# Performance work log

Measured on AMD Instinct MI355X. Metric: run time of the kernel, lower is better.

## Reference

```python
import jax, jax.numpy as jnp
import numpy as np

N_NODES = 50000
N_EDGES = 600000
IN_F = 128
OUT_F = 128
SMALL = max(IN_F // 10, 1)  # floor(128/10) = 12
D_K = np.sqrt(SMALL).astype(np.float32)


def setup_inputs() -> dict:
    key = jax.random.key(0)
    ks = jax.random.split(key, 10)
    node_data = jax.random.normal(ks[0], (N_NODES, IN_F), dtype=jnp.float32)
    src = jax.random.randint(ks[1], (N_EDGES,), 0, N_NODES, dtype=jnp.int32)
    dst = jax.random.randint(ks[2], (N_EDGES,), 0, N_NODES, dtype=jnp.int32)
    s_q = 1.0 / np.sqrt(IN_F)
    Wq = jax.random.uniform(ks[3], (SMALL, IN_F), jnp.float32, -s_q, s_q)
    bq = jax.random.uniform(ks[4], (SMALL,), jnp.float32, -s_q, s_q)
    Wk = jax.random.uniform(ks[5], (SMALL, IN_F), jnp.float32, -s_q, s_q)
    bk = jax.random.uniform(ks[6], (SMALL,), jnp.float32, -s_q, s_q)
    W1 = jax.random.uniform(ks[7], (OUT_F, IN_F), jnp.float32, -s_q, s_q)
    W2 = jax.random.uniform(ks[8], (OUT_F, IN_F), jnp.float32, -s_q, s_q)
    b2 = jax.random.uniform(ks[9], (OUT_F,), jnp.float32, -s_q, s_q)
    return {"node_data": node_data, "src": src, "dst": dst,
            "Wq": Wq, "bq": bq, "Wk": Wk, "bk": bk,
            "W1": W1, "W2": W2, "b2": b2}


def reference(node_data, src, dst, Wq, bq, Wk, bk, W1, W2, b2):
    N = node_data.shape[0]
    # dgl.add_self_loop: append (i, i) for every node -> each dst has >= 1 edge
    loops = jnp.arange(N, dtype=src.dtype)
    s = jnp.concatenate([src, loops])
    d = jnp.concatenate([dst, loops])

    # query = Tanh(Linear), key = Linear  (shapes [N, SMALL])
    q = jnp.tanh(node_data @ Wq.T + bq)
    k = node_data @ Wk.T + bk

    # per-edge score: sum(query[src] * key[dst]) / sqrt(small)
    scores = jnp.sum(q[s] * k[d], axis=1) / D_K  # [E]

    # softmax over incoming edges of each dst node (segment softmax)
    seg_max = jax.ops.segment_max(scores, d, num_segments=N)
    w = jnp.exp(scores - seg_max[d])
    seg_sum = jax.ops.segment_sum(w, d, num_segments=N)
    w = w / seg_sum[d]  # [E]

    # weighted scatter-aggregate of src node inputs -> [N, IN_F]
    att = jax.ops.segment_sum(w[:, None] * node_data[s], d, num_segments=N)

    # DeepSetLayer: layer1(node_data) + layer2(node attention)
    x = node_data @ W1.T + (att @ W2.T + b2)
    # per-row L2 ('fro' over dim=1) normalization, then ReLU
    x = x / jnp.linalg.norm(x, axis=1, keepdims=True)
    return jax.nn.relu(x)
```

## Files before the change

kernel.cpp:

```cpp
#include <hip/hip_runtime.h>
#include <hip/hip_bf16.h>
#include <math.h>
#include <stdint.h>


#define IN_F 128
#define SMALL 12
#define QK_PAD 16
#define BUCKET 64

typedef __attribute__((ext_vector_type(8))) _Float16 half8;
typedef __attribute__((ext_vector_type(8))) unsigned short ushort8;
typedef __attribute__((ext_vector_type(4))) float f32x4;
typedef __attribute__((ext_vector_type(2))) float floatx2;

__device__ __forceinline__ float dot12(const float* __restrict__ qrow,
                                       float4 c0, float4 c1, float4 c2) {
    float4 a = ((const float4*)qrow)[0];
    float4 b = ((const float4*)qrow)[1];
    float4 c = ((const float4*)qrow)[2];
    return a.x*c0.x + a.y*c0.y + a.z*c0.z + a.w*c0.w
         + b.x*c1.x + b.y*c1.y + b.z*c1.z + b.w*c1.w
         + c.x*c2.x + c.y*c2.y + c.z*c2.z + c.w*c2.w;
}

__device__ __forceinline__ half8 ld_h8(const float* p) {
    float4 x0 = *(const float4*)p;
    float4 x1 = *(const float4*)(p + 4);
    half8 a;
    a[0] = (_Float16)x0.x; a[1] = (_Float16)x0.y;
    a[2] = (_Float16)x0.z; a[3] = (_Float16)x0.w;
    a[4] = (_Float16)x1.x; a[5] = (_Float16)x1.y;
    a[6] = (_Float16)x1.z; a[7] = (_Float16)x1.w;
    return a;
}

__global__ __launch_bounds__(256) void prep_kernel(
    const float* __restrict__ nd,
    const float* __restrict__ Wq, const float* __restrict__ bq,
    const float* __restrict__ Wk, const float* __restrict__ bk,
    const int* __restrict__ src, const int* __restrict__ dst,
    const float* __restrict__ W1, const float* __restrict__ W2,
    float* __restrict__ q, float* __restrict__ kf,
    unsigned short* __restrict__ ndb, unsigned char* __restrict__ nd8,
    int* __restrict__ cnt, unsigned short* __restrict__ esrc,
    unsigned short* __restrict__ Wc,
    int N, int E, int NBQK, int NBCNT)
{
    int t = threadIdx.x;
    int b = blockIdx.x;

    if (b < NBQK) {
        int wv = t >> 6;
        int lane = t & 63;
        int col = lane & 15;
        int quad = lane >> 4;
        int tbase = b * 64 + wv * 16;

        int arow = tbase + col;
        int rowc = (arow < N) ? arow : (N - 1);
        const float* ap = nd + (size_t)rowc * IN_F + quad * 8;
        unsigned short* np = ndb + (size_t)arow * IN_F + quad * 8;
        unsigned char* n8p = nd8 + (size_t)arow * IN_F + quad * 8;

        const float* w0 = ((col < 12) ? (Wq + (size_t)col * IN_F)
                                      : (Wk + (size_t)(col - 12) * IN_F)) + quad * 8;
        const float* w1 = Wk + (size_t)((col < 8) ? (col + 4) : 4) * IN_F + quad * 8;
        bool hasw1 = (col < 8);

        half8 zero = {};
        f32x4 acc0 = (f32x4)0.f, acc1 = (f32x4)0.f;
#pragma unroll
        for (int ks = 0; ks < 4; ks++) {
            int k0 = ks * 32;
            float4 x0 = *(const float4*)(ap + k0);
            float4 x1 = *(const float4*)(ap + k0 + 4);
            half8 a;
            a[0] = (_Float16)x0.x; a[1] = (_Float16)x0.y;
            a[2] = (_Float16)x0.z; a[3] = (_Float16)x0.w;
            a[4] = (_Float16)x1.x; a[5] = (_Float16)x1.y;
            a[6] = (_Float16)x1.z; a[7] = (_Float16)x1.w;
            if (arow < N) {
                *(half8*)(np + k0) = a;
                int p0 = __builtin_amdgcn_cvt_pk_fp8_f32(x0.x, x0.y, 0, false);
                p0 = __builtin_amdgcn_cvt_pk_fp8_f32(x0.z, x0.w, p0, true);
                int p1 = __builtin_amdgcn_cvt_pk_fp8_f32(x1.x, x1.y, 0, false);
                p1 = __builtin_amdgcn_cvt_pk_fp8_f32(x1.z, x1.w, p1, true);
                uint2 pv; pv.x = (unsigned)p0; pv.y = (unsigned)p1;
                *(uint2*)(n8p + k0) = pv;
            }
            half8 bb0 = ld_h8(w0 + k0);
            half8 bb1 = hasw1 ? ld_h8(w1 + k0) : zero;
            acc0 = __builtin_amdgcn_mfma_f32_16x16x32_f16(a, bb0, acc0, 0, 0, 0);
            acc1 = __builtin_amdgcn_mfma_f32_16x16x32_f16(a, bb1, acc1, 0, 0, 0);
        }
        float bias0 = (col < 12) ? bq[col] : bk[col - 12];
        float bias1 = (col < 8) ? bk[col + 4] : 0.f;
#pragma unroll
        for (int r = 0; r < 4; r++) {
            int node = tbase + quad * 4 + r;
            if (node < N) {
                float v0 = acc0[r] + bias0;
                if (col < 12) q[(size_t)node * QK_PAD + col] = tanhf(v0);
                else          kf[(size_t)node * QK_PAD + (col - 12)] = v0;
                if (hasw1)    kf[(size_t)node * QK_PAD + col + 4] = acc1[r] + bias1;
            }
        }
    } else if (b < NBQK + NBCNT) {
        int ET = E + N;
        int stride = NBCNT * 256;
        for (int i = (b - NBQK) * 256 + t; i < ET; i += stride) {
            int d, s;
            if (i < E) { d = dst[i]; s = src[i]; }
            else       { d = i - E; s = d; }
            int pos = atomicAdd(&cnt[d], 1);
            if (pos < BUCKET)
                esrc[(size_t)d * BUCKET + pos] = (unsigned short)s;
        }
    } else {
        int idx = (b - NBQK - NBCNT) * 256 + t;
        int f = idx >> 8, k = idx & 255;
        float v = (k < 128) ? W1[f * 128 + k] : W2[f * 128 + (k - 128)];
        ((_Float16*)Wc)[idx] = (_Float16)v;
    }
}

__global__ __launch_bounds__(256) void attn_kernel(
    const unsigned short* __restrict__ ndb, const unsigned char* __restrict__ nd8,
    const float* __restrict__ q,
    const float* __restrict__ kf,
    const int* __restrict__ cnt, const unsigned short* __restrict__ esrc,
    void* __restrict__ attv, int att16, int N)
{
    const float INVDK = 0.28867513459481287f;
    int t = threadIdx.x;
    int lane = t & 63;
    int l16 = lane & 15;
    int gbase = lane & 48;
    int wid = blockIdx.x * 16 + (t >> 4);
    if (wid >= N) return;

    int start = wid * BUCKET;
    int deg = cnt[wid];
    if (deg > BUCKET) deg = BUCKET;

    const float4* kp = (const float4*)(kf + (size_t)wid * QK_PAD);
    float4 c0 = kp[0], c1 = kp[1], c2 = kp[2];

    float acc[8];
#pragma unroll
    for (int j = 0; j < 8; j++) acc[j] = 0.f;
    float inv;

    const unsigned short* nb = ndb + l16 * 8;
    const unsigned char* nb8 = nd8 + l16 * 8;

#define ACCUM(hv, ww) do {                                                    \
        acc[0] += (ww) * (float)(hv)[0]; acc[1] += (ww) * (float)(hv)[1];     \
        acc[2] += (ww) * (float)(hv)[2]; acc[3] += (ww) * (float)(hv)[3];     \
        acc[4] += (ww) * (float)(hv)[4]; acc[5] += (ww) * (float)(hv)[5];     \
        acc[6] += (ww) * (float)(hv)[6]; acc[7] += (ww) * (float)(hv)[7];     \
    } while (0)

#define ACCUMQ(pv, ww) do {                                                   \
        floatx2 f0 = __builtin_amdgcn_cvt_pk_f32_fp8((int)(pv).x, false);     \
        floatx2 f1 = __builtin_amdgcn_cvt_pk_f32_fp8((int)(pv).x, true);      \
        floatx2 f2 = __builtin_amdgcn_cvt_pk_f32_fp8((int)(pv).y, false);     \
        floatx2 f3 = __builtin_amdgcn_cvt_pk_f32_fp8((int)(pv).y, true);      \
        acc[0] += (ww) * f0[0]; acc[1] += (ww) * f0[1];                       \
        acc[2] += (ww) * f1[0]; acc[3] += (ww) * f1[1];                       \
        acc[4] += (ww) * f2[0]; acc[5] += (ww) * f2[1];                       \
        acc[6] += (ww) * f3[0]; acc[7] += (ww) * f3[1]; } while (0)

#define LOAD8Q(pfx, id)                                                       \
    uint2 pfx##0 = *(const uint2*)(nb8 + (size_t)(id)[0] * IN_F);             \
    uint2 pfx##1 = *(const uint2*)(nb8 + (size_t)(id)[1] * IN_F);             \
    uint2 pfx##2 = *(const uint2*)(nb8 + (size_t)(id)[2] * IN_F);             \
    uint2 pfx##3 = *(const uint2*)(nb8 + (size_t)(id)[3] * IN_F);             \
    uint2 pfx##4 = *(const uint2*)(nb8 + (size_t)(id)[4] * IN_F);             \
    uint2 pfx##5 = *(const uint2*)(nb8 + (size_t)(id)[5] * IN_F);             \
    uint2 pfx##6 = *(const uint2*)(nb8 + (size_t)(id)[6] * IN_F);             \
    uint2 pfx##7 = *(const uint2*)(nb8 + (size_t)(id)[7] * IN_F)

#define SHFL8(wsrc, base)                                                     \
    do { _Pragma("unroll")                                                    \
         for (int _i = 0; _i < 8; _i++) wa[_i] = __shfl((wsrc), gbase | ((base) + _i)); } while (0)

#define ACCUM8Q(pfx) do {                                                     \
        ACCUMQ(pfx##0, wa[0]); ACCUMQ(pfx##1, wa[1]);                         \
        ACCUMQ(pfx##2, wa[2]); ACCUMQ(pfx##3, wa[3]);                         \
        ACCUMQ(pfx##4, wa[4]); ACCUMQ(pfx##5, wa[5]);                         \
        ACCUMQ(pfx##6, wa[6]); ACCUMQ(pfx##7, wa[7]); } while (0)

    if (deg <= 32) {
        ushort8 pk0 = *(const ushort8*)(esrc + start);
        ushort8 pk1 = *(const ushort8*)(esrc + start + 8);

        int id0[8];
#pragma unroll
        for (int i = 0; i < 8; i++) id0[i] = (i < deg) ? (int)pk0[i] : 0;
        LOAD8Q(v, id0);

        int si = (int)esrc[start + l16];
        float sc = -INFINITY;
        if (l16 < deg)
            sc = dot12(q + (size_t)si * QK_PAD, c0, c1, c2) * INVDK;
        float sc1 = -INFINITY;
        if (deg > 16) {
            int si1 = (int)esrc[start + 16 + l16];
            if (16 + l16 < deg)
                sc1 = dot12(q + (size_t)si1 * QK_PAD, c0, c1, c2) * INVDK;
        }
        float m = fmaxf(sc, sc1);
#pragma unroll
        for (int o = 8; o > 0; o >>= 1) m = fmaxf(m, __shfl_xor(m, o));
        float w  = (l16 < deg)      ? __expf(sc - m)  : 0.f;
        float w1 = (16 + l16 < deg) ? __expf(sc1 - m) : 0.f;
        float ls = w + w1;
#pragma unroll
        for (int o = 8; o > 0; o >>= 1) ls += __shfl_xor(ls, o);
        inv = 1.f / ls;

        int id1[8];
#pragma unroll
        for (int i = 0; i < 8; i++) id1[i] = (8 + i < deg) ? (int)pk1[i] : 0;
        LOAD8Q(u, id1);

        float wa[8];
        SHFL8(w, 0);
        ACCUM8Q(v);
        SHFL8(w, 8);
        ACCUM8Q(u);

        if (deg > 16) {
            ushort8 pk2 = *(const ushort8*)(esrc + start + 16);
            ushort8 pk3 = *(const ushort8*)(esrc + start + 24);
            int id2[8], id3[8];
#pragma unroll
            for (int i = 0; i < 8; i++) id2[i] = (16 + i < deg) ? (int)pk2[i] : 0;
#pragma unroll
            for (int i = 0; i < 8; i++) id3[i] = (24 + i < deg) ? (int)pk3[i] : 0;
            LOAD8Q(x, id2);
            LOAD8Q(y, id3);
            SHFL8(w1, 0);
            ACCUM8Q(x);
            SHFL8(w1, 8);
            ACCUM8Q(y);
        }
    } else {
        float m = -INFINITY;
        for (int i = l16; i < deg; i += 16) {
            int s2 = (int)esrc[start + i];
            m = fmaxf(m, dot12(q + (size_t)s2 * QK_PAD, c0, c1, c2) * INVDK);
        }
#pragma unroll
        for (int o = 8; o > 0; o >>= 1) m = fmaxf(m, __shfl_xor(m, o));
        float ls = 0.f;
        for (int i = l16; i < deg; i += 16) {
            int s2 = (int)esrc[start + i];
            ls += __expf(dot12(q + (size_t)s2 * QK_PAD, c0, c1, c2) * INVDK - m);
        }
#pragma unroll
        for (int o = 8; o > 0; o >>= 1) ls += __shfl_xor(ls, o);
        inv = 1.f / ls;

        for (int base2 = 0; base2 < deg; base2 += 16) {
            int cnt2 = deg - base2; if (cnt2 > 16) cnt2 = 16;
            float w = 0.f; int si = 0;
            if (l16 < cnt2) {
                si = (int)esrc[start + base2 + l16];
                w = __expf(dot12(q + (size_t)si * QK_PAD, c0, c1, c2) * INVDK - m);
            }
            int i = 0;
            for (; i + 4 <= cnt2; i += 4) {
                float u0 = __shfl(w, gbase | i);       int s0 = __shfl(si, gbase | i);
                float u1 = __shfl(w, gbase | (i + 1)); int s1 = __shfl(si, gbase | (i + 1));
                float u2 = __shfl(w, gbase | (i + 2)); int s2 = __shfl(si, gbase | (i + 2));
                float u3 = __shfl(w, gbase | (i + 3)); int s3 = __shfl(si, gbase | (i + 3));
                half8 x0 = *(const half8*)(nb + (size_t)s0 * IN_F);
                half8 x1 = *(const half8*)(nb + (size_t)s1 * IN_F);
                half8 x2 = *(const half8*)(nb + (size_t)s2 * IN_F);
                half8 x3 = *(const half8*)(nb + (size_t)s3 * IN_F);
                ACCUM(x0, u0); ACCUM(x1, u1); ACCUM(x2, u2); ACCUM(x3, u3);
            }
            for (; i < cnt2; i++) {
                float wi = __shfl(w, gbase | i);
                int ri = __shfl(si, gbase | i);
                half8 x = *(const half8*)(nb + (size_t)ri * IN_F);
                ACCUM(x, wi);
            }
        }
    }
#undef ACCUM8Q
#undef SHFL8
#undef LOAD8Q
#undef ACCUMQ
#undef ACCUM

    if (att16) {
        unsigned short* op = (unsigned short*)attv + (size_t)wid * IN_F + l16 * 8;
        half8 st;
#pragma unroll
        for (int j = 0; j < 8; j++) st[j] = (_Float16)(acc[j] * inv);
        *(half8*)op = st;
    } else {
        float* op = (float*)attv + (size_t)wid * IN_F + l16 * 8;
        float4 s0, s1;
        s0.x = acc[0] * inv; s0.y = acc[1] * inv; s0.z = acc[2] * inv; s0.w = acc[3] * inv;
        s1.x = acc[4] * inv; s1.y = acc[5] * inv; s1.z = acc[6] * inv; s1.w = acc[7] * inv;
        *(float4*)op = s0;
        *(float4*)(op + 4) = s1;
    }
}

__global__ __launch_bounds__(256) void final_kernel(
    const unsigned short* __restrict__ ndb, const float* __restrict__ nd,
    const void* __restrict__ attv, int att16,
    const unsigned short* __restrict__ Wc, const float* __restrict__ b2,
    float* __restrict__ out, int N)
{
    int wv = threadIdx.x >> 6;
    int lane = threadIdx.x & 63;
    int col = lane & 15;
    int quad = lane >> 4;

    int arow = blockIdx.x * 64 + wv * 16 + col;
    int rowc = (arow < N) ? arow : (N - 1);
    const unsigned short* a0p = ndb + (size_t)rowc * IN_F + quad * 8;
    const unsigned short* a1h = (const unsigned short*)attv + (size_t)rowc * IN_F + quad * 8;
    const float* a1f = ((arow < N) ? (const float*)attv : nd) + (size_t)rowc * IN_F + quad * 8;

    f32x4 acc[8];
#pragma unroll
    for (int i = 0; i < 8; i++) acc[i] = (f32x4)0.f;

#pragma unroll
    for (int ks = 0; ks < 8; ks++) {
        int k0 = ks * 32;
        half8 a;
        if (ks < 4)      a = *(const half8*)(a0p + k0);
        else if (att16)  a = *(const half8*)(a1h + (k0 - 128));
        else             a = ld_h8(a1f + (k0 - 128));
#pragma unroll
        for (int ft = 0; ft < 8; ft++) {
            int n = ft * 16 + col;
            half8 bb = *(const half8*)(Wc + (size_t)n * 256 + k0 + quad * 8);
            acc[ft] = __builtin_amdgcn_mfma_f32_16x16x32_f16(a, bb, acc[ft], 0, 0, 0);
        }
    }

    float bias[8];
#pragma unroll
    for (int ft = 0; ft < 8; ft++) bias[ft] = b2[ft * 16 + col];

#pragma unroll
    for (int r = 0; r < 4; r++) {
        int node = blockIdx.x * 64 + wv * 16 + quad * 4 + r;
        float v[8];
        float ps = 0.f;
#pragma unroll
        for (int ft = 0; ft < 8; ft++) {
            v[ft] = acc[ft][r] + bias[ft];
            ps += v[ft] * v[ft];
        }
        ps += __shfl_xor(ps, 1);
        ps += __shfl_xor(ps, 2);
        ps += __shfl_xor(ps, 4);
        ps += __shfl_xor(ps, 8);
        float rn = rsqrtf(ps);
        if (node < N) {
            float* op = out + (size_t)node * 128 + col;
#pragma unroll
            for (int ft = 0; ft < 8; ft++)
                op[ft * 16] = fmaxf(v[ft] * rn, 0.f);
        }
    }
}

static inline char* align_up(char* p, size_t a) {
    return (char*)(((uintptr_t)p + (a - 1)) & ~(uintptr_t)(a - 1));
}

extern "C" void kernel_launch(void* const* d_in, const int* in_sizes, int n_in,
                              void* d_out, int out_size, void* d_ws, size_t ws_size,
                              hipStream_t stream) {
    const float* node_data = (const float*)d_in[0];
    const int*   src       = (const int*)d_in[1];
    const int*   dst       = (const int*)d_in[2];
    const float* Wq        = (const float*)d_in[3];
    const float* bq        = (const float*)d_in[4];
    const float* Wk        = (const float*)d_in[5];
    const float* bk        = (const float*)d_in[6];
    const float* W1        = (const float*)d_in[7];
    const float* W2        = (const float*)d_in[8];
    const float* b2        = (const float*)d_in[9];
    float* out = (float*)d_out;

    int N = in_sizes[0] / IN_F;
    int E = in_sizes[1];
    int NBQK = (N + 63) / 64;
    int NBCNT = 512;
    int NBCVT = 128;

    char* w = (char*)d_ws;
    float* q  = (float*)w;  w += (size_t)N * QK_PAD * sizeof(float);
    float* kf = (float*)w;  w += (size_t)N * QK_PAD * sizeof(float);
    w = align_up(w, 256);
    unsigned short* ndb = (unsigned short*)w;  w += (size_t)N * IN_F * sizeof(unsigned short);
    w = align_up(w, 256);
    unsigned char* nd8 = (unsigned char*)w;  w += (size_t)N * IN_F;
    w = align_up(w, 256);
    unsigned short* Wc = (unsigned short*)w;  w += 128 * 256 * sizeof(unsigned short);
    int* cnt  = (int*)w;  w += (size_t)N * sizeof(int);
    w = align_up(w, 256);
    unsigned short* esrc = (unsigned short*)w;  w += (size_t)N * BUCKET * sizeof(unsigned short);

    w = align_up(w, 256);
    int att16 = 0;
    void* attp = out;
    if ((size_t)(w - (char*)d_ws) + (size_t)N * IN_F * sizeof(unsigned short) <= ws_size) {
        att16 = 1;
        attp = w;
    }

    hipMemsetAsync(cnt, 0, (size_t)N * sizeof(int), stream);

    prep_kernel<<<NBQK + NBCNT + NBCVT, 256, 0, stream>>>(
        node_data, Wq, bq, Wk, bk, src, dst, W1, W2,
        q, kf, ndb, nd8, cnt, esrc, Wc, N, E, NBQK, NBCNT);
    attn_kernel<<<(N + 15) / 16, 256, 0, stream>>>(ndb, nd8, q, kf, cnt, esrc, attp, att16, N);
    final_kernel<<<(N + 63) / 64, 256, 0, stream>>>(ndb, node_data, attp, att16, Wc, b2, out, N);
}
```

Baseline: 189.7 us.

## Synthesize self-loop edges implicitly and schedule atomic bucketing blocks first

Self-loop edges are no longer pushed through the atomic bucketing pass; instead attn_kernel treats one extra slot past the real degree as the node itself. The counting/bucketing blocks are moved to the front of prep_kernel's grid and doubled in number so the atomic-heavy work is dispatched earlier and with more parallelism. This removes N atomics and scatter writes, at the cost of extra per-index selects in the attention kernel. The bucket capacity now effectively includes one more slot, and edge order differs slightly from before.

```diff
diff --git a/kernel.cpp b/kernel.cpp
--- a/kernel.cpp
+++ b/kernel.cpp
@@ -50,12 +50,22 @@
     int t = threadIdx.x;
     int b = blockIdx.x;
 
-    if (b < NBQK) {
+    if (b < NBCNT) {
+        int stride = NBCNT * 256;
+        for (int i = b * 256 + t; i < E; i += stride) {
+            int d = dst[i];
+            int s = src[i];
+            int pos = atomicAdd(&cnt[d], 1);
+            if (pos < BUCKET)
+                esrc[(size_t)d * BUCKET + pos] = (unsigned short)s;
+        }
+    } else if (b < NBCNT + NBQK) {
+        int bq2 = b - NBCNT;
         int wv = t >> 6;
         int lane = t & 63;
         int col = lane & 15;
         int quad = lane >> 4;
-        int tbase = b * 64 + wv * 16;
+        int tbase = bq2 * 64 + wv * 16;
 
         int arow = tbase + col;
         int rowc = (arow < N) ? arow : (N - 1);
@@ -106,19 +116,8 @@
                 if (hasw1)    kf[(size_t)node * QK_PAD + col + 4] = acc1[r] + bias1;
             }
         }
-    } else if (b < NBQK + NBCNT) {
-        int ET = E + N;
-        int stride = NBCNT * 256;
-        for (int i = (b - NBQK) * 256 + t; i < ET; i += stride) {
-            int d, s;
-            if (i < E) { d = dst[i]; s = src[i]; }
-            else       { d = i - E; s = d; }
-            int pos = atomicAdd(&cnt[d], 1);
-            if (pos < BUCKET)
-                esrc[(size_t)d * BUCKET + pos] = (unsigned short)s;
-        }
     } else {
-        int idx = (b - NBQK - NBCNT) * 256 + t;
+        int idx = (b - NBCNT - NBQK) * 256 + t;
         int f = idx >> 8, k = idx & 255;
         float v = (k < 128) ? W1[f * 128 + k] : W2[f * 128 + (k - 128)];
         ((_Float16*)Wc)[idx] = (_Float16)v;
@@ -141,8 +140,9 @@
     if (wid >= N) return;
 
     int start = wid * BUCKET;
-    int deg = cnt[wid];
-    if (deg > BUCKET) deg = BUCKET;
+    int degR = cnt[wid];
+    if (degR > BUCKET) degR = BUCKET;
+    int deg = degR + 1;
 
     const float4* kp = (const float4*)(kf + (size_t)wid * QK_PAD);
     float4 c0 = kp[0], c1 = kp[1], c2 = kp[2];
@@ -198,16 +198,16 @@
 
         int id0[8];
 #pragma unroll
-        for (int i = 0; i < 8; i++) id0[i] = (i < deg) ? (int)pk0[i] : 0;
+        for (int i = 0; i < 8; i++) id0[i] = (i < degR) ? (int)pk0[i] : wid;
         LOAD8Q(v, id0);
 
-        int si = (int)esrc[start + l16];
+        int si = (l16 < degR) ? (int)esrc[start + l16] : wid;
         float sc = -INFINITY;
         if (l16 < deg)
             sc = dot12(q + (size_t)si * QK_PAD, c0, c1, c2) * INVDK;
         float sc1 = -INFINITY;
         if (deg > 16) {
-            int si1 = (int)esrc[start + 16 + l16];
+            int si1 = (16 + l16 < degR) ? (int)esrc[start + 16 + l16] : wid;
             if (16 + l16 < deg)
                 sc1 = dot12(q + (size_t)si1 * QK_PAD, c0, c1, c2) * INVDK;
         }
@@ -223,7 +223,7 @@
 
         int id1[8];
 #pragma unroll
-        for (int i = 0; i < 8; i++) id1[i] = (8 + i < deg) ? (int)pk1[i] : 0;
+        for (int i = 0; i < 8; i++) id1[i] = (8 + i < degR) ? (int)pk1[i] : wid;
         LOAD8Q(u, id1);
 
         float wa[8];
@@ -237,9 +237,9 @@
             ushort8 pk3 = *(const ushort8*)(esrc + start + 24);
             int id2[8], id3[8];
 #pragma unroll
-            for (int i = 0; i < 8; i++) id2[i] = (16 + i < deg) ? (int)pk2[i] : 0;
-#pragma unroll
-            for (int i = 0; i < 8; i++) id3[i] = (24 + i < deg) ? (int)pk3[i] : 0;
+            for (int i = 0; i < 8; i++) id2[i] = (16 + i < degR) ? (int)pk2[i] : wid;
+#pragma unroll
+            for (int i = 0; i < 8; i++) id3[i] = (24 + i < degR) ? (int)pk3[i] : wid;
             LOAD8Q(x, id2);
             LOAD8Q(y, id3);
             SHFL8(w1, 0);
@@ -250,14 +250,14 @@
     } else {
         float m = -INFINITY;
         for (int i = l16; i < deg; i += 16) {
-            int s2 = (int)esrc[start + i];
+            int s2 = (i < degR) ? (int)esrc[start + i] : wid;
             m = fmaxf(m, dot12(q + (size_t)s2 * QK_PAD, c0, c1, c2) * INVDK);
         }
 #pragma unroll
         for (int o = 8; o > 0; o >>= 1) m = fmaxf(m, __shfl_xor(m, o));
         float ls = 0.f;
         for (int i = l16; i < deg; i += 16) {
-            int s2 = (int)esrc[start + i];
+            int s2 = (i < degR) ? (int)esrc[start + i] : wid;
             ls += __expf(dot12(q + (size_t)s2 * QK_PAD, c0, c1, c2) * INVDK - m);
         }
 #pragma unroll
@@ -268,7 +268,7 @@
             int cnt2 = deg - base2; if (cnt2 > 16) cnt2 = 16;
             float w = 0.f; int si = 0;
             if (l16 < cnt2) {
-                si = (int)esrc[start + base2 + l16];
+                si = (base2 + l16 < degR) ? (int)esrc[start + base2 + l16] : wid;
                 w = __expf(dot12(q + (size_t)si * QK_PAD, c0, c1, c2) * INVDK - m);
             }
             int i = 0;
@@ -399,7 +399,7 @@
     int N = in_sizes[0] / IN_F;
     int E = in_sizes[1];
     int NBQK = (N + 63) / 64;
-    int NBCNT = 512;
+    int NBCNT = 1024;
     int NBCVT = 128;
 
     char* w = (char*)d_ws;
@@ -425,9 +425,9 @@
 
     hipMemsetAsync(cnt, 0, (size_t)N * sizeof(int), stream);
 
-    prep_kernel<<<NBQK + NBCNT + NBCVT, 256, 0, stream>>>(
+    prep_kernel<<<NBCNT + NBQK + NBCVT, 256, 0, stream>>>(
         node_data, Wq, bq, Wk, bk, src, dst, W1, W2,
         q, kf, ndb, nd8, cnt, esrc, Wc, N, E, NBQK, NBCNT);
     attn_kernel<<<(N + 15) / 16, 256, 0, stream>>>(ndb, nd8, q, kf, cnt, esrc, attp, att16, N);
-    final_kernel<<<(N + 63) / 64, 256, 0, stream>>>(ndb, node_data, attp, att16, Wc, b2, out, N);
-}
+    final_kernel<<<(N + 63) / 64, 256, 0, stream>>>(ndb, nd8 ? node_data : node_data, attp, att16, Wc, b2, out, N);
+}
```

Measured after the change: 199.6 us. 5.2% more time.
